# Performance work log

Hardware: AMD Instinct MI355X
Metric: run time of the kernel (lower is better)

The kernel has to match this reference:

```python
import jax, jax.numpy as jnp
import numpy as np
import math

Z_DIM = 128
N_HEAD = 4
C = 32
L = 512


def setup_inputs() -> dict:
    key = jax.random.key(0)
    ks = jax.random.split(key, 16)
    s = lambda fan_in: 1.0 / math.sqrt(fan_in)
    hc = N_HEAD * C
    return {
        "z_": jax.random.normal(ks[0], (L, L, Z_DIM), dtype=jnp.float32),
        "ln_g": jnp.ones((Z_DIM,), jnp.float32),
        "ln_b": jnp.zeros((Z_DIM,), jnp.float32),
        "qw": jax.random.normal(ks[1], (Z_DIM, hc), jnp.float32) * s(Z_DIM),
        "qb": jnp.zeros((hc,), jnp.float32),
        "kw": jax.random.normal(ks[2], (Z_DIM, hc), jnp.float32) * s(Z_DIM),
        "kb": jnp.zeros((hc,), jnp.float32),
        "vw": jax.random.normal(ks[3], (Z_DIM, hc), jnp.float32) * s(Z_DIM),
        "vb": jnp.zeros((hc,), jnp.float32),
        "bw": jax.random.normal(ks[4], (Z_DIM, N_HEAD), jnp.float32) * s(Z_DIM),
        "bb": jnp.zeros((N_HEAD,), jnp.float32),
        "gw": jax.random.normal(ks[5], (Z_DIM, hc), jnp.float32) * s(Z_DIM),
        "gb": jnp.zeros((hc,), jnp.float32),
        "ow": jax.random.normal(ks[6], (hc, Z_DIM), jnp.float32) * s(hc),
        "ob": jnp.zeros((Z_DIM,), jnp.float32),
    }


def _layernorm(x, g, b, eps=1e-5):
    mu = jnp.mean(x, axis=-1, keepdims=True)
    var = jnp.var(x, axis=-1, keepdims=True)
    return (x - mu) * jax.lax.rsqrt(var + eps) * g + b


def reference(z_, ln_g, ln_b, qw, qb, kw, kb, vw, vb, bw, bb, gw, gb, ow, ob):
    L1, L2, D = z_.shape
    z = _layernorm(z_, ln_g, ln_b)
    q = (z @ qw + qb).reshape(L1, L2, N_HEAD, C)
    k = (z @ kw + kb).reshape(L1, L2, N_HEAD, C)
    v = (z @ vw + vb).reshape(L1, L2, N_HEAD, C)
    bias = z @ bw + bb  # [L1, L2, H]
    scale = (1.0 / math.sqrt(C)) / math.sqrt(L2)
    # Note: reduction over the leading (row) axis b, per the source einsum.
    att = jnp.einsum('blhc,bkhc->lkh', q, k) * scale + bias  # [L, L, H]
    att = jax.nn.softmax(att, axis=1)
    o = jnp.einsum('lkh,bkhc->blhc', att, v)  # [L1, L2, H, C]
    g = jax.nn.sigmoid((z @ gw + gb).reshape(L1, L2, N_HEAD, C))
    o = (g * o).reshape(L1, L2, N_HEAD * C)
    return o @ ow + ob
```

## Files before the change

### kernel.cpp

```cpp
#include <hip/hip_runtime.h>
#include <hip/hip_bf16.h>
#include <math.h>


#define LL 512
#define ZD 128
#define NROWS (LL*LL)
#define ATT_SCALE (1.0f/128.0f)
#define NSPLIT 8

typedef __attribute__((ext_vector_type(4))) float f32x4;
typedef __attribute__((ext_vector_type(8))) short short8;
typedef __attribute__((ext_vector_type(8))) unsigned short u16x8;

__device__ __forceinline__ unsigned short f2bf(float f){
  union { float f; unsigned u; } v; v.f = f;
  unsigned r = (v.u + 0x7FFFu + ((v.u >> 16) & 1u)) >> 16;
  return (unsigned short)r;
}
__device__ __forceinline__ float bf2f(unsigned short h){
  union { float f; unsigned u; } v; v.u = ((unsigned)h) << 16;
  return v.f;
}

__global__ void k_prep(const float* __restrict__ qw, const float* __restrict__ kw,
                       const float* __restrict__ vw, const float* __restrict__ gw,
                       const float* __restrict__ bw,
                       const float* __restrict__ qb, const float* __restrict__ kb,
                       const float* __restrict__ vb, const float* __restrict__ gb,
                       const float* __restrict__ bb,
                       const float* __restrict__ ow,
                       unsigned short* __restrict__ Wt, unsigned short* __restrict__ Ot,
                       float* __restrict__ biasv){
  int n = blockIdx.x;
  int k = threadIdx.x;
  if (n < 516){
    float v;
    if (n < 128)      v = qw[k*128 + n];
    else if (n < 256) v = kw[k*128 + (n-128)];
    else if (n < 384) v = vw[k*128 + (n-256)];
    else if (n < 512) v = gw[k*128 + (n-384)];
    else              v = bw[k*4   + (n-512)];
    Wt[n*ZD + k] = f2bf(v);
    if (k == 0){
      float bvv;
      if (n < 128)      bvv = qb[n];
      else if (n < 256) bvv = kb[n-128];
      else if (n < 384) bvv = vb[n-256];
      else if (n < 512) bvv = gb[n-384];
      else              bvv = bb[n-512];
      biasv[n] = bvv;
    }
  } else {
    int d = n - 516;
    Ot[d*ZD + k] = f2bf(ow[k*ZD + d]);
  }
}

__launch_bounds__(256, 3)
__global__ void k_proj(const float* __restrict__ z,
                       const float* __restrict__ ln_g, const float* __restrict__ ln_b,
                       const unsigned short* __restrict__ Wt,
                       const float* __restrict__ biasv,
                       unsigned short* __restrict__ proj,
                       float* __restrict__ biasz){
  const int P = 136;
  __shared__ unsigned short As[128*136];
  __shared__ float lng[128], lnb[128];
  __shared__ float lbias[640];
  int t = threadIdx.x;
  long mbase = (long)blockIdx.x * 128;
  if (t < 128){ lng[t] = ln_g[t]; lnb[t] = ln_b[t]; }
  if (t < 160) *(float4*)&lbias[t*4] = *(const float4*)&biasv[t*4];
  {
    int row = t >> 1, half = t & 1;
    const float4* zr = (const float4*)(z + (mbase + row)*ZD + half*64);
    float4 zv[16];
    float s1 = 0.f, s2 = 0.f;
#pragma unroll
    for (int i = 0; i < 16; i++){
      zv[i] = zr[i];
      s1 += zv[i].x + zv[i].y + zv[i].z + zv[i].w;
      s2 += zv[i].x*zv[i].x + zv[i].y*zv[i].y + zv[i].z*zv[i].z + zv[i].w*zv[i].w;
    }
    s1 += __shfl_xor(s1, 1);
    s2 += __shfl_xor(s2, 1);
    float mu = s1 * (1.f/128.f);
    float rs = rsqrtf(s2*(1.f/128.f) - mu*mu + 1e-5f);
    __syncthreads();
#pragma unroll
    for (int i = 0; i < 16; i++){
      int c0 = half*64 + i*4;
      ushort4 pk;
      pk.x = f2bf((zv[i].x - mu)*rs*lng[c0+0] + lnb[c0+0]);
      pk.y = f2bf((zv[i].y - mu)*rs*lng[c0+1] + lnb[c0+1]);
      pk.z = f2bf((zv[i].z - mu)*rs*lng[c0+2] + lnb[c0+2]);
      pk.w = f2bf((zv[i].w - mu)*rs*lng[c0+3] + lnb[c0+3]);
      *(ushort4*)&As[row*P + c0] = pk;
    }
  }
  __syncthreads();
  int w = t >> 6, tl = t & 63;
  int m0 = (w & 1)*64, n0 = (w >> 1)*64;
  int lr = tl & 15, quad = tl >> 4;
  for (int nt = 0; nt < 5; nt++){
    f32x4 acc[4][4];
    for (int i=0;i<4;i++) for (int j=0;j<4;j++) acc[i][j] = f32x4{0.f,0.f,0.f,0.f};
    for (int kk = 0; kk < 4; kk++){
      short8 a[4], bq[4];
      for (int i=0;i<4;i++) a[i] = *(const short8*)&As[(m0 + i*16 + lr)*P + kk*32 + quad*8];
      const unsigned short* wp = Wt + ((long)nt*128 + n0 + lr)*ZD + kk*32 + quad*8;
      for (int j=0;j<4;j++) bq[j] = *(const short8*)(wp + (long)j*16*ZD);
      for (int i=0;i<4;i++) for (int j=0;j<4;j++)
        acc[i][j] = __builtin_amdgcn_mfma_f32_16x16x32_bf16(bq[j], a[i], acc[i][j], 0,0,0);
    }
    if (nt < 4){
      float4 bd[4];
#pragma unroll
      for (int j=0;j<4;j++) bd[j] = *(const float4*)&lbias[nt*128 + n0 + j*16 + quad*4];
#pragma unroll
      for (int i=0;i<4;i++){
        long grow = mbase + m0 + i*16 + lr;
#pragma unroll
        for (int j=0;j<4;j++){
          int nc0 = n0 + j*16 + quad*4;
          ushort4 pk;
          pk.x = f2bf(acc[i][j][0] + bd[j].x);
          pk.y = f2bf(acc[i][j][1] + bd[j].y);
          pk.z = f2bf(acc[i][j][2] + bd[j].z);
          pk.w = f2bf(acc[i][j][3] + bd[j].w);
          *(ushort4*)&proj[grow*512 + nt*128 + nc0] = pk;
        }
      }
    } else if (n0 == 0 && quad == 0){
      float4 bd = *(const float4*)&lbias[512];
#pragma unroll
      for (int i=0;i<4;i++){
        long grow = mbase + m0 + i*16 + lr;
        float4 o;
        o.x = acc[i][0][0] + bd.x;
        o.y = acc[i][0][1] + bd.y;
        o.z = acc[i][0][2] + bd.z;
        o.w = acc[i][0][3] + bd.w;
        *(float4*)&biasz[grow*4] = o;
      }
    }
  }
}

__launch_bounds__(256, 2)
__global__ void k_att(const unsigned short* __restrict__ proj,
                      float* __restrict__ partial){
  const int P = 40;
  __shared__ unsigned short As[128*40];
  __shared__ unsigned short Bs[128*40];
  int t = threadIdx.x;
  int ktb = blockIdx.x * 128, ltb = blockIdx.y * 128;
  int split = blockIdx.z >> 2, h = blockIdx.z & 3;
  int w = t >> 6, tl = t & 63;
  int m0 = (w & 1)*64, n0 = (w >> 1)*64;
  int lr = tl & 15, quad = tl >> 4;
  int srow = t >> 1, shalf = t & 1;
  f32x4 acc[4][4];
  for (int i=0;i<4;i++) for (int j=0;j<4;j++) acc[i][j] = f32x4{0.f,0.f,0.f,0.f};
  for (int it = 0; it < 64; it++){
    int b = split*64 + it;
    long abase = ((long)b*LL + ltb + srow)*512 +       h*32 + shalf*16;
    long bbase = ((long)b*LL + ktb + srow)*512 + 128 + h*32 + shalf*16;
    u16x8 av0 = *(const u16x8*)&proj[abase];
    u16x8 av1 = *(const u16x8*)&proj[abase + 8];
    u16x8 bv0 = *(const u16x8*)&proj[bbase];
    u16x8 bv1 = *(const u16x8*)&proj[bbase + 8];
    __syncthreads();
    *(u16x8*)&As[srow*P + shalf*16]     = av0;
    *(u16x8*)&As[srow*P + shalf*16 + 8] = av1;
    *(u16x8*)&Bs[srow*P + shalf*16]     = bv0;
    *(u16x8*)&Bs[srow*P + shalf*16 + 8] = bv1;
    __syncthreads();
    short8 a[4], bq[4];
    for (int i=0;i<4;i++) a[i]  = *(const short8*)&As[(m0 + i*16 + lr)*P + quad*8];
    for (int i=0;i<4;i++) bq[i] = *(const short8*)&Bs[(n0 + i*16 + lr)*P + quad*8];
    for (int i=0;i<4;i++) for (int j=0;j<4;j++)
      acc[i][j] = __builtin_amdgcn_mfma_f32_16x16x32_bf16(a[i], bq[j], acc[i][j], 0,0,0);
  }
  long obase = (((long)(split*4 + h)*LL) + ltb)*512 + ktb;
  for (int i=0;i<4;i++) for (int j=0;j<4;j++){
    int ncol = n0 + j*16 + lr;
    for (int r=0;r<4;r++){
      int mrow = m0 + i*16 + quad*4 + r;
      partial[obase + (long)mrow*512 + ncol] = acc[i][j][r];
    }
  }
}

__global__ void k_soft(const float* __restrict__ partial,
                       const float* __restrict__ biasz,
                       unsigned short* __restrict__ attb){
  int bx = blockIdx.x;
  int h = bx >> 9, l = bx & 511;
  int t = threadIdx.x;
  int k1 = t, k2 = t + 256;
  float v1 = 0.f, v2 = 0.f;
  for (int s = 0; s < NSPLIT; s++){
    long base = (((long)(s*4 + h)*LL) + l)*512;
    v1 += partial[base + k1];
    v2 += partial[base + k2];
  }
  v1 = v1*ATT_SCALE + biasz[((long)l*512 + k1)*4 + h];
  v2 = v2*ATT_SCALE + biasz[((long)l*512 + k2)*4 + h];
  __shared__ float red[4];
  int w = t >> 6, tl = t & 63;
  float mx = fmaxf(v1, v2);
  for (int o = 32; o > 0; o >>= 1) mx = fmaxf(mx, __shfl_xor(mx, o));
  if (tl == 0) red[w] = mx;
  __syncthreads();
  mx = fmaxf(fmaxf(red[0], red[1]), fmaxf(red[2], red[3]));
  __syncthreads();
  float e1 = __expf(v1 - mx), e2 = __expf(v2 - mx);
  float sm = e1 + e2;
  for (int o = 32; o > 0; o >>= 1) sm += __shfl_xor(sm, o);
  if (tl == 0) red[w] = sm;
  __syncthreads();
  sm = red[0] + red[1] + red[2] + red[3];
  float inv = 1.f / sm;
  long ob = ((long)h*LL + l)*512;
  attb[ob + k1] = f2bf(e1*inv);
  attb[ob + k2] = f2bf(e2*inv);
}

__launch_bounds__(256, 2)
__global__ void k_o(const unsigned short* __restrict__ attb,
                    const unsigned short* __restrict__ proj,
                    unsigned short* __restrict__ xbuf){
  const int P = 40;
  __shared__ unsigned short As[4*128*40];
  __shared__ unsigned short Bs[4*32*40];
  int t = threadIdx.x;
  int ltb = blockIdx.x * 128;
  int b   = blockIdx.y;
  int w = t >> 6, tl = t & 63;
  int lr = tl & 15, quad = tl >> 4;
  f32x4 acc[8][2];
  for (int i=0;i<8;i++) for (int j=0;j<2;j++) acc[i][j] = f32x4{0.f,0.f,0.f,0.f};
  for (int it = 0; it < 16; it++){
    int kb = it*32;
    long a0 = (((long)w*LL) + ltb + tl)*512 + kb;
    long a1 = a0 + 64L*512;
    u16x8 r0[4], r1[4];
    for (int i=0;i<4;i++) r0[i] = *(const u16x8*)&attb[a0 + i*8];
    for (int i=0;i<4;i++) r1[i] = *(const u16x8*)&attb[a1 + i*8];
    int kp = tl >> 1, hc2 = tl & 1;
    long vbs = ((long)b*LL + kb + kp)*512 + 256 + w*32 + hc2*16;
    u16x8 v0 = *(const u16x8*)&proj[vbs];
    u16x8 v1 = *(const u16x8*)&proj[vbs + 8];
    __syncthreads();
    for (int i=0;i<4;i++) *(u16x8*)&As[(w*128 + tl)*P + i*8]      = r0[i];
    for (int i=0;i<4;i++) *(u16x8*)&As[(w*128 + tl + 64)*P + i*8] = r1[i];
    for (int j=0;j<8;j++){
      Bs[(w*32 + hc2*16 + j    )*P + kp] = v0[j];
      Bs[(w*32 + hc2*16 + 8 + j)*P + kp] = v1[j];
    }
    __syncthreads();
    short8 a[8], bq[2];
    for (int i=0;i<8;i++) a[i]  = *(const short8*)&As[(w*128 + i*16 + lr)*P + quad*8];
    for (int j=0;j<2;j++) bq[j] = *(const short8*)&Bs[(w*32  + j*16 + lr)*P + quad*8];
    for (int i=0;i<8;i++) for (int j=0;j<2;j++)
      acc[i][j] = __builtin_amdgcn_mfma_f32_16x16x32_bf16(a[i], bq[j], acc[i][j], 0,0,0);
  }
  for (int i=0;i<8;i++) for (int j=0;j<2;j++) for (int r=0;r<4;r++){
    int l = i*16 + quad*4 + r;
    int c = j*16 + lr;
    long grow = (long)b*LL + ltb + l;
    float gv = bf2f(proj[grow*512 + 384 + w*32 + c]);
    float sg = 1.f / (1.f + __expf(-gv));
    xbuf[grow*128 + w*32 + c] = f2bf(acc[i][j][r] * sg);
  }
}

__launch_bounds__(256, 2)
__global__ void k_fin(const unsigned short* __restrict__ xbuf,
                      const unsigned short* __restrict__ Ot,
                      const float* __restrict__ ob,
                      float* __restrict__ out){
  const int P = 136;
  __shared__ unsigned short As[128*136];
  __shared__ unsigned short Bs[128*136];
  int t = threadIdx.x;
  long mbase = (long)blockIdx.x * 128;
  {
    int row = t >> 1, half = t & 1;
    const u16x8* src = (const u16x8*)(xbuf + (mbase + row)*128 + half*64);
    u16x8* dst = (u16x8*)&As[row*P + half*64];
    for (int i=0;i<8;i++) dst[i] = src[i];
    const u16x8* wsrc = (const u16x8*)(Ot + row*128 + half*64);
    u16x8* wdst = (u16x8*)&Bs[row*P + half*64];
    for (int i=0;i<8;i++) wdst[i] = wsrc[i];
  }
  __syncthreads();
  int w = t >> 6, tl = t & 63;
  int m0 = (w & 1)*64, n0 = (w >> 1)*64;
  int lr = tl & 15, quad = tl >> 4;
  f32x4 acc[4][4];
  for (int i=0;i<4;i++) for (int j=0;j<4;j++) acc[i][j] = f32x4{0.f,0.f,0.f,0.f};
  for (int kk = 0; kk < 4; kk++){
    short8 a[4], bq[4];
    for (int i=0;i<4;i++) a[i]  = *(const short8*)&As[(m0 + i*16 + lr)*P + kk*32 + quad*8];
    for (int i=0;i<4;i++) bq[i] = *(const short8*)&Bs[(n0 + i*16 + lr)*P + kk*32 + quad*8];
    for (int i=0;i<4;i++) for (int j=0;j<4;j++)
      acc[i][j] = __builtin_amdgcn_mfma_f32_16x16x32_bf16(a[i], bq[j], acc[i][j], 0,0,0);
  }
  for (int i=0;i<4;i++) for (int j=0;j<4;j++){
    int ncol = n0 + j*16 + lr;
    float bv = ob[ncol];
    for (int r=0;r<4;r++){
      int mrow = m0 + i*16 + quad*4 + r;
      out[(mbase + mrow)*128 + ncol] = acc[i][j][r] + bv;
    }
  }
}

extern "C" void kernel_launch(void* const* d_in, const int* in_sizes, int n_in,
                              void* d_out, int out_size, void* d_ws, size_t ws_size,
                              hipStream_t stream){
  (void)in_sizes; (void)n_in; (void)out_size; (void)ws_size;
  const float* z    = (const float*)d_in[0];
  const float* ln_g = (const float*)d_in[1];
  const float* ln_b = (const float*)d_in[2];
  const float* qw   = (const float*)d_in[3];
  const float* qb   = (const float*)d_in[4];
  const float* kw   = (const float*)d_in[5];
  const float* kb   = (const float*)d_in[6];
  const float* vw   = (const float*)d_in[7];
  const float* vb   = (const float*)d_in[8];
  const float* bw   = (const float*)d_in[9];
  const float* bb   = (const float*)d_in[10];
  const float* gw   = (const float*)d_in[11];
  const float* gb   = (const float*)d_in[12];
  const float* ow   = (const float*)d_in[13];
  const float* ob   = (const float*)d_in[14];
  float* out = (float*)d_out;

  char* wsp = (char*)d_ws;
  unsigned short* Wt    = (unsigned short*)(wsp);
  unsigned short* Ot    = (unsigned short*)(wsp + 163840);
  float*          biasv = (float*)(wsp + 196608);
  unsigned short* proj  = (unsigned short*)(wsp + 262144);
  char* xreg = wsp + 262144 + 268435456L;
  float*          partial = (float*)xreg;
  float*          biasz   = (float*)(xreg + 33554432L);
  unsigned short* xbuf    = (unsigned short*)xreg;
  unsigned short* attb    = (unsigned short*)(xreg + 67108864L);

  k_prep<<<644, 128, 0, stream>>>(qw,kw,vw,gw,bw,qb,kb,vb,gb,bb,ow,Wt,Ot,biasv);
  k_proj<<<2048, 256, 0, stream>>>(z, ln_g, ln_b, Wt, biasv, proj, biasz);
  k_att<<<dim3(4,4,32), 256, 0, stream>>>(proj, partial);
  k_soft<<<2048, 256, 0, stream>>>(partial, biasz, attb);
  k_o<<<dim3(4,512), 256, 0, stream>>>(attb, proj, xbuf);
  k_fin<<<2048, 256, 0, stream>>>(xbuf, Ot, ob, out);
}
```

Baseline: 667.2 us.

## Split projection buffer into Q/K/G planes plus transposed V, drop LDS staging

The single interleaved projection buffer is replaced by separate Q, K and gate buffers with 128-wide rows and a per-batch transposed V buffer written directly from the MFMA accumulator layout. k_att and k_o now load MFMA operands straight from global memory instead of staging through shared memory with two barriers per iteration, and their occupancy hints rise to three blocks. This removes LDS traffic, barriers and the scalar V transpose in k_o. In exchange, operand reuse across waves now depends on L1/L2 cache rather than LDS, and the projection kernel does strided transposed stores for V.

```diff
diff --git a/kernel.cpp b/kernel.cpp
--- a/kernel.cpp
+++ b/kernel.cpp
@@ -62,7 +62,10 @@
                        const float* __restrict__ ln_g, const float* __restrict__ ln_b,
                        const unsigned short* __restrict__ Wt,
                        const float* __restrict__ biasv,
-                       unsigned short* __restrict__ proj,
+                       unsigned short* __restrict__ qbuf,
+                       unsigned short* __restrict__ kbuf,
+                       unsigned short* __restrict__ vt,
+                       unsigned short* __restrict__ gbuf,
                        float* __restrict__ biasz){
   const int P = 136;
   __shared__ unsigned short As[128*136];
@@ -70,6 +73,8 @@
   __shared__ float lbias[640];
   int t = threadIdx.x;
   long mbase = (long)blockIdx.x * 128;
+  int bb_ = (int)(mbase >> 9);
+  int rr0 = (int)(mbase & 511);
   if (t < 128){ lng[t] = ln_g[t]; lnb[t] = ln_b[t]; }
   if (t < 160) *(float4*)&lbias[t*4] = *(const float4*)&biasv[t*4];
   {
@@ -103,6 +108,7 @@
   int w = t >> 6, tl = t & 63;
   int m0 = (w & 1)*64, n0 = (w >> 1)*64;
   int lr = tl & 15, quad = tl >> 4;
+#pragma unroll
   for (int nt = 0; nt < 5; nt++){
     f32x4 acc[4][4];
     for (int i=0;i<4;i++) for (int j=0;j<4;j++) acc[i][j] = f32x4{0.f,0.f,0.f,0.f};
@@ -111,10 +117,13 @@
       for (int i=0;i<4;i++) a[i] = *(const short8*)&As[(m0 + i*16 + lr)*P + kk*32 + quad*8];
       const unsigned short* wp = Wt + ((long)nt*128 + n0 + lr)*ZD + kk*32 + quad*8;
       for (int j=0;j<4;j++) bq[j] = *(const short8*)(wp + (long)j*16*ZD);
-      for (int i=0;i<4;i++) for (int j=0;j<4;j++)
-        acc[i][j] = __builtin_amdgcn_mfma_f32_16x16x32_bf16(bq[j], a[i], acc[i][j], 0,0,0);
-    }
-    if (nt < 4){
+      for (int i=0;i<4;i++) for (int j=0;j<4;j++){
+        if (nt == 2) acc[i][j] = __builtin_amdgcn_mfma_f32_16x16x32_bf16(a[i], bq[j], acc[i][j], 0,0,0);
+        else         acc[i][j] = __builtin_amdgcn_mfma_f32_16x16x32_bf16(bq[j], a[i], acc[i][j], 0,0,0);
+      }
+    }
+    if (nt == 0 || nt == 1 || nt == 3){
+      unsigned short* dst = (nt == 0) ? qbuf : (nt == 1) ? kbuf : gbuf;
       float4 bd[4];
 #pragma unroll
       for (int j=0;j<4;j++) bd[j] = *(const float4*)&lbias[nt*128 + n0 + j*16 + quad*4];
@@ -129,7 +138,23 @@
           pk.y = f2bf(acc[i][j][1] + bd[j].y);
           pk.z = f2bf(acc[i][j][2] + bd[j].z);
           pk.w = f2bf(acc[i][j][3] + bd[j].w);
-          *(ushort4*)&proj[grow*512 + nt*128 + nc0] = pk;
+          *(ushort4*)&dst[grow*128 + nc0] = pk;
+        }
+      }
+    } else if (nt == 2){
+#pragma unroll
+      for (int j=0;j<4;j++){
+        int ncol = n0 + j*16 + lr;
+        float bv = lbias[256 + ncol];
+#pragma unroll
+        for (int i=0;i<4;i++){
+          int rr = rr0 + m0 + i*16 + quad*4;
+          ushort4 pk;
+          pk.x = f2bf(acc[i][j][0] + bv);
+          pk.y = f2bf(acc[i][j][1] + bv);
+          pk.z = f2bf(acc[i][j][2] + bv);
+          pk.w = f2bf(acc[i][j][3] + bv);
+          *(ushort4*)&vt[((long)bb_*128 + ncol)*512 + rr] = pk;
         }
       }
     } else if (n0 == 0 && quad == 0){
@@ -148,38 +173,28 @@
   }
 }
 
-__launch_bounds__(256, 2)
-__global__ void k_att(const unsigned short* __restrict__ proj,
+__launch_bounds__(256, 3)
+__global__ void k_att(const unsigned short* __restrict__ qbuf,
+                      const unsigned short* __restrict__ kbuf,
                       float* __restrict__ partial){
-  const int P = 40;
-  __shared__ unsigned short As[128*40];
-  __shared__ unsigned short Bs[128*40];
   int t = threadIdx.x;
   int ktb = blockIdx.x * 128, ltb = blockIdx.y * 128;
   int split = blockIdx.z >> 2, h = blockIdx.z & 3;
   int w = t >> 6, tl = t & 63;
   int m0 = (w & 1)*64, n0 = (w >> 1)*64;
   int lr = tl & 15, quad = tl >> 4;
-  int srow = t >> 1, shalf = t & 1;
   f32x4 acc[4][4];
   for (int i=0;i<4;i++) for (int j=0;j<4;j++) acc[i][j] = f32x4{0.f,0.f,0.f,0.f};
   for (int it = 0; it < 64; it++){
     int b = split*64 + it;
-    long abase = ((long)b*LL + ltb + srow)*512 +       h*32 + shalf*16;
-    long bbase = ((long)b*LL + ktb + srow)*512 + 128 + h*32 + shalf*16;
-    u16x8 av0 = *(const u16x8*)&proj[abase];
-    u16x8 av1 = *(const u16x8*)&proj[abase + 8];
-    u16x8 bv0 = *(const u16x8*)&proj[bbase];
-    u16x8 bv1 = *(const u16x8*)&proj[bbase + 8];
-    __syncthreads();
-    *(u16x8*)&As[srow*P + shalf*16]     = av0;
-    *(u16x8*)&As[srow*P + shalf*16 + 8] = av1;
-    *(u16x8*)&Bs[srow*P + shalf*16]     = bv0;
-    *(u16x8*)&Bs[srow*P + shalf*16 + 8] = bv1;
-    __syncthreads();
+    long qb0 = ((long)b*LL + ltb + m0 + lr)*128 + h*32 + quad*8;
+    long kb0 = ((long)b*LL + ktb + n0 + lr)*128 + h*32 + quad*8;
     short8 a[4], bq[4];
-    for (int i=0;i<4;i++) a[i]  = *(const short8*)&As[(m0 + i*16 + lr)*P + quad*8];
-    for (int i=0;i<4;i++) bq[i] = *(const short8*)&Bs[(n0 + i*16 + lr)*P + quad*8];
+#pragma unroll
+    for (int i=0;i<4;i++) a[i]  = *(const short8*)&qbuf[qb0 + (long)i*16*128];
+#pragma unroll
+    for (int i=0;i<4;i++) bq[i] = *(const short8*)&kbuf[kb0 + (long)i*16*128];
+#pragma unroll
     for (int i=0;i<4;i++) for (int j=0;j<4;j++)
       acc[i][j] = __builtin_amdgcn_mfma_f32_16x16x32_bf16(a[i], bq[j], acc[i][j], 0,0,0);
   }
@@ -228,13 +243,11 @@
   attb[ob + k2] = f2bf(e2*inv);
 }
 
-__launch_bounds__(256, 2)
+__launch_bounds__(256, 3)
 __global__ void k_o(const unsigned short* __restrict__ attb,
-                    const unsigned short* __restrict__ proj,
+                    const unsigned short* __restrict__ vt,
+                    const unsigned short* __restrict__ gbuf,
                     unsigned short* __restrict__ xbuf){
-  const int P = 40;
-  __shared__ unsigned short As[4*128*40];
-  __shared__ unsigned short Bs[4*32*40];
   int t = threadIdx.x;
   int ltb = blockIdx.x * 128;
   int b   = blockIdx.y;
@@ -242,28 +255,16 @@
   int lr = tl & 15, quad = tl >> 4;
   f32x4 acc[8][2];
   for (int i=0;i<8;i++) for (int j=0;j<2;j++) acc[i][j] = f32x4{0.f,0.f,0.f,0.f};
+  long abase0 = ((long)w*LL + ltb + lr)*512;
+  long vbase0 = ((long)b*128 + w*32 + lr)*512;
   for (int it = 0; it < 16; it++){
-    int kb = it*32;
-    long a0 = (((long)w*LL) + ltb + tl)*512 + kb;
-    long a1 = a0 + 64L*512;
-    u16x8 r0[4], r1[4];
-    for (int i=0;i<4;i++) r0[i] = *(const u16x8*)&attb[a0 + i*8];
-    for (int i=0;i<4;i++) r1[i] = *(const u16x8*)&attb[a1 + i*8];
-    int kp = tl >> 1, hc2 = tl & 1;
-    long vbs = ((long)b*LL + kb + kp)*512 + 256 + w*32 + hc2*16;
-    u16x8 v0 = *(const u16x8*)&proj[vbs];
-    u16x8 v1 = *(const u16x8*)&proj[vbs + 8];
-    __syncthreads();
-    for (int i=0;i<4;i++) *(u16x8*)&As[(w*128 + tl)*P + i*8]      = r0[i];
-    for (int i=0;i<4;i++) *(u16x8*)&As[(w*128 + tl + 64)*P + i*8] = r1[i];
-    for (int j=0;j<8;j++){
-      Bs[(w*32 + hc2*16 + j    )*P + kp] = v0[j];
-      Bs[(w*32 + hc2*16 + 8 + j)*P + kp] = v1[j];
-    }
-    __syncthreads();
+    int kb = it*32 + quad*8;
     short8 a[8], bq[2];
-    for (int i=0;i<8;i++) a[i]  = *(const short8*)&As[(w*128 + i*16 + lr)*P + quad*8];
-    for (int j=0;j<2;j++) bq[j] = *(const short8*)&Bs[(w*32  + j*16 + lr)*P + quad*8];
+#pragma unroll
+    for (int i=0;i<8;i++) a[i]  = *(const short8*)&attb[abase0 + (long)i*16*512 + kb];
+#pragma unroll
+    for (int j=0;j<2;j++) bq[j] = *(const short8*)&vt[vbase0 + (long)j*16*512 + kb];
+#pragma unroll
     for (int i=0;i<8;i++) for (int j=0;j<2;j++)
       acc[i][j] = __builtin_amdgcn_mfma_f32_16x16x32_bf16(a[i], bq[j], acc[i][j], 0,0,0);
   }
@@ -271,7 +272,7 @@
     int l = i*16 + quad*4 + r;
     int c = j*16 + lr;
     long grow = (long)b*LL + ltb + l;
-    float gv = bf2f(proj[grow*512 + 384 + w*32 + c]);
+    float gv = bf2f(gbuf[grow*128 + w*32 + c]);
     float sg = 1.f / (1.f + __expf(-gv));
     xbuf[grow*128 + w*32 + c] = f2bf(acc[i][j][r] * sg);
   }
@@ -344,17 +345,20 @@
   unsigned short* Wt    = (unsigned short*)(wsp);
   unsigned short* Ot    = (unsigned short*)(wsp + 163840);
   float*          biasv = (float*)(wsp + 196608);
-  unsigned short* proj  = (unsigned short*)(wsp + 262144);
-  char* xreg = wsp + 262144 + 268435456L;
+  unsigned short* qbuf  = (unsigned short*)(wsp + 262144);
+  unsigned short* kbuf  = (unsigned short*)(wsp + 262144 + 67108864L);
+  unsigned short* vt    = (unsigned short*)(wsp + 262144 + 2*67108864L);
+  unsigned short* gbuf  = (unsigned short*)(wsp + 262144 + 3*67108864L);
+  char* xreg = wsp + 262144 + 4*67108864L;
   float*          partial = (float*)xreg;
   float*          biasz   = (float*)(xreg + 33554432L);
   unsigned short* xbuf    = (unsigned short*)xreg;
   unsigned short* attb    = (unsigned short*)(xreg + 67108864L);
 
   k_prep<<<644, 128, 0, stream>>>(qw,kw,vw,gw,bw,qb,kb,vb,gb,bb,ow,Wt,Ot,biasv);
-  k_proj<<<2048, 256, 0, stream>>>(z, ln_g, ln_b, Wt, biasv, proj, biasz);
-  k_att<<<dim3(4,4,32), 256, 0, stream>>>(proj, partial);
+  k_proj<<<2048, 256, 0, stream>>>(z, ln_g, ln_b, Wt, biasv, qbuf, kbuf, vt, gbuf, biasz);
+  k_att<<<dim3(4,4,32), 256, 0, stream>>>(qbuf, kbuf, partial);
   k_soft<<<2048, 256, 0, stream>>>(partial, biasz, attb);
-  k_o<<<dim3(4,512), 256, 0, stream>>>(attb, proj, xbuf);
+  k_o<<<dim3(4,512), 256, 0, stream>>>(attb, vt, gbuf, xbuf);
   k_fin<<<2048, 256, 0, stream>>>(xbuf, Ot, ob, out);
 }
```

After: 735.3 us. 10.2% more time.
